# Optimization experiments

Hardware: AMD Instinct MI355X
Metric: run time of the kernel (lower is better)

## Reference

```python
import jax, jax.numpy as jnp
import numpy as np

NEG = -1e30  # finite stand-in for log(0); safe for logaddexp and its gradient


def setup_inputs() -> dict:
    key = jax.random.key(0)
    k1, k2 = jax.random.split(key)
    B, T, C, U = 256, 512, 128, 128
    logits = jax.random.normal(k1, (B, T, C), dtype=jnp.float32)
    y_pred = jax.nn.softmax(logits, axis=-1)  # ctc_batch_cost expects probabilities
    y_true = jax.random.randint(k2, (B, U), 0, C - 1)  # labels exclude blank=C-1
    return {"y_true": y_true, "y_pred": y_pred}


def _ctc_batch_cost(y_true, y_pred):
    """Keras-style CTC: blank = num_classes-1, logp = log(y_pred + 1e-7),
    full input_length = T and label_length = U for every row (as in the layer).
    Returns loss of shape [B, 1]."""
    B, T, C = y_pred.shape
    U = y_true.shape[1]
    blank = C - 1
    S = 2 * U + 1  # extended label: blank-interleaved
    logp = jnp.log(y_pred + 1e-7)  # [B,T,C], keras epsilon

    # extended label sequence z = [blank, l1, blank, l2, ..., lU, blank]
    ext = jnp.full((B, S), blank, dtype=y_true.dtype).at[:, 1::2].set(y_true)

    # lp[t,b,s] = logp[b,t,ext[b,s]]
    lp = jnp.take_along_axis(logp, jnp.broadcast_to(ext[:, None, :], (B, T, S)), axis=2)
    lp = jnp.transpose(lp, (1, 0, 2))  # [T,B,S]

    # skip transition s-2 -> s allowed iff z[s] != blank and z[s] != z[s-2]
    ext_m2 = jnp.pad(ext, ((0, 0), (2, 0)), constant_values=blank)[:, :S]
    skip = (ext != blank) & (ext != ext_m2)
    skip = skip.at[:, :2].set(False)  # no s-2 predecessor for s in {0,1}

    alpha0 = jnp.full((B, S), NEG, dtype=logp.dtype)
    alpha0 = alpha0.at[:, 0].set(lp[0, :, 0]).at[:, 1].set(lp[0, :, 1])

    def step(a, lp_t):
        a1 = jnp.pad(a, ((0, 0), (1, 0)), constant_values=NEG)[:, :S]
        a2 = jnp.pad(a, ((0, 0), (2, 0)), constant_values=NEG)[:, :S]
        a2 = jnp.where(skip, a2, NEG)
        a = jnp.logaddexp(jnp.logaddexp(a, a1), a2) + lp_t
        return a, None

    aT, _ = jax.lax.scan(step, alpha0, lp[1:])
    loss = -jnp.logaddexp(aT[:, S - 1], aT[:, S - 2])
    return loss[:, None]  # [B,1], matching ctc_batch_cost output shape


def reference(y_true, y_pred):
    # The layer returns y_pred and registers the loss via add_loss; the loss is
    # the actual computation of interest, so we return it.
    return _ctc_batch_cost(y_true, y_pred)
```

## Files before the change

kernel.cpp:

```cpp
#include <hip/hip_runtime.h>

#define EPSF 1e-7f

#define DPPF0(x, ctrl) \
    __int_as_float(__builtin_amdgcn_update_dpp(0, __float_as_int(x), ctrl, 0xF, 0xF, false))

__device__ __forceinline__ float f_rcp(float x) { return __builtin_amdgcn_rcpf(x); }
__device__ __forceinline__ float wave_shr1_f(float x) { return DPPF0(x, 0x138); }

__device__ __forceinline__ float wave_max64(float x) {
    x = fmaxf(x, DPPF0(x, 0x111));
    x = fmaxf(x, DPPF0(x, 0x112));
    x = fmaxf(x, DPPF0(x, 0x114));
    x = fmaxf(x, DPPF0(x, 0x118));
    x = fmaxf(x, DPPF0(x, 0x142));
    x = fmaxf(x, DPPF0(x, 0x143));
    return __int_as_float(__builtin_amdgcn_readlane(__float_as_int(x), 63));
}

#define SB0() __builtin_amdgcn_sched_barrier(0)
#define WAITV(N) do { asm volatile("s_waitcnt vmcnt(" #N ")" ::: "memory"); SB0(); } while (0)

#define ISS(dst, voff, IMM) \
    asm volatile("global_load_dword %0, %1, %2 offset:" #IMM \
                 : "=v"(dst) : "v"(voff), "s"(pn))

#define ISSUE_W8(X) do { \
    ISS(X##b[0], vb, 0);    ISS(X##l1[0], v1, 0);    ISS(X##l3[0], v3, 0); \
    ISS(X##b[1], vb, 512);  ISS(X##l1[1], v1, 512);  ISS(X##l3[1], v3, 512); \
    ISS(X##b[2], vb, 1024); ISS(X##l1[2], v1, 1024); ISS(X##l3[2], v3, 1024); \
    ISS(X##b[3], vb, 1536); ISS(X##l1[3], v1, 1536); ISS(X##l3[3], v3, 1536); \
    ISS(X##b[4], vb, 2048); ISS(X##l1[4], v1, 2048); ISS(X##l3[4], v3, 2048); \
    ISS(X##b[5], vb, 2560); ISS(X##l1[5], v1, 2560); ISS(X##l3[5], v3, 2560); \
    ISS(X##b[6], vb, 3072); ISS(X##l1[6], v1, 3072); ISS(X##l3[6], v3, 3072); \
    ISS(X##b[7], vb, 3584); ISS(X##l1[7], v1, 3584); ISS(X##l3[7], v3, 3584); \
    pn += 8 * 128; \
} while (0)

#define ISSUE_W7(X) do { \
    ISS(X##b[0], vb, 0);    ISS(X##l1[0], v1, 0);    ISS(X##l3[0], v3, 0); \
    ISS(X##b[1], vb, 512);  ISS(X##l1[1], v1, 512);  ISS(X##l3[1], v3, 512); \
    ISS(X##b[2], vb, 1024); ISS(X##l1[2], v1, 1024); ISS(X##l3[2], v3, 1024); \
    ISS(X##b[3], vb, 1536); ISS(X##l1[3], v1, 1536); ISS(X##l3[3], v3, 1536); \
    ISS(X##b[4], vb, 2048); ISS(X##l1[4], v1, 2048); ISS(X##l3[4], v3, 2048); \
    ISS(X##b[5], vb, 2560); ISS(X##l1[5], v1, 2560); ISS(X##l3[5], v3, 2560); \
    ISS(X##b[6], vb, 3072); ISS(X##l1[6], v1, 3072); ISS(X##l3[6], v3, 3072); \
} while (0)

#define STEP(PB_, P1_, P3_) do { \
    const float pbe = (PB_) + EPSF; \
    const float rpb = f_rcp(pbe); \
    const float q1  = ((P1_) + EPSF) * rpb; \
    const float q3  = ((P3_) + EPSF) * rpb; \
    const float n3  = wave_shr1_f(u3); \
    const float t1  = fmaf(m1, n3, u0 + u1); \
    const float t3  = fmaf(m3, u1, u2 + u3); \
    u4 = u4 + u3; \
    u3 = t3 * q3; \
    u2 = u2 + u1; \
    u1 = t1 * q1; \
    u0 = u0 + n3; \
    O += __logf(pbe); \
} while (0)

#define APPLY() do { \
    const float rm_ = f_rcp(m_carry); \
    u0 *= rm_; u1 *= rm_; u2 *= rm_; u3 *= rm_; u4 *= rm_; \
    O += __logf(m_carry); \
} while (0)

#define SNAP() do { \
    m_carry = wave_max64(fmaxf(fmaxf(u0, u1), fmaxf(u2, fmaxf(u3, u4)))); \
} while (0)

#define STEPK(X, k) STEP(X##b[k], X##l1[k], X##l3[k])
#define CONSUME_W8(X) do { \
    STEPK(X,0); STEPK(X,1); APPLY(); \
    STEPK(X,2); STEPK(X,3); STEPK(X,4); STEPK(X,5); STEPK(X,6); STEPK(X,7); \
    SNAP(); \
} while (0)
#define CONSUME_T7(X) do { \
    STEPK(X,0); STEPK(X,1); APPLY(); \
    STEPK(X,2); STEPK(X,3); STEPK(X,4); STEPK(X,5); STEPK(X,6); \
} while (0)

__global__ __launch_bounds__(64, 1) void ctc_pipe512(
        const int* __restrict__ y_true, const float* __restrict__ y_pred,
        float* __restrict__ out) {
    const int b    = blockIdx.x;
    const int lane = threadIdx.x;
    const float* __restrict__ yp = y_pred + (size_t)b * (512 * 128);

    const int2 lc = ((const int2*)(y_true + (size_t)b * 128))[lane];
    const int c1 = lc.x, c3 = lc.y;
    const int cp = __builtin_amdgcn_update_dpp(0, c3, 0x138, 0xF, 0xF, false);
    const float m1 = (lane > 0 && c1 != cp) ? 1.f : 0.f;
    const float m3 = (c3 != c1) ? 1.f : 0.f;

    float u0, u1, u2 = 0.f, u3 = 0.f, u4 = 0.f;
    {
        const float pvb = yp[127];
        const float pv1 = yp[c1];
        u0 = (lane == 0) ? pvb + EPSF : 0.f;
        u1 = (lane == 0) ? pv1 + EPSF : 0.f;
    }
    float O = 0.f, m_carry = 1.0f;

    const int vb = 127 * 4;
    const int v1 = c1 * 4;
    const int v3 = c3 * 4;
    const float* pn = yp + 128;

    WAITV(0);

    float Ab[8], Al1[8], Al3[8];
    float Bb[8], Bl1[8], Bl3[8];
    float Cb[8], Cl1[8], Cl3[8];

    ISSUE_W8(A);
    ISSUE_W8(B);

    for (int j = 0; j < 20; ++j) {
        ISSUE_W8(C);  WAITV(48);  CONSUME_W8(A);
        ISSUE_W8(A);  WAITV(48);  CONSUME_W8(B);
        ISSUE_W8(B);  WAITV(48);  CONSUME_W8(C);
    }
    ISSUE_W8(C);
    WAITV(48);  CONSUME_W8(A);
    ISSUE_W7(A);
    WAITV(45);  CONSUME_W8(B);
    WAITV(21);  CONSUME_W8(C);
    WAITV(0);   CONSUME_T7(A);

    if (lane == 63) out[b] = -(O + __logf(u3 + u4));
}

__global__ __launch_bounds__(64, 1) void ctc_scan_generic(
        const int* __restrict__ y_true, const float* __restrict__ y_pred,
        float* __restrict__ out, int T, int C, int U) {
    const int b    = blockIdx.x;
    const int lane = threadIdx.x;
    const int blank = C - 1;
    const float* __restrict__ yp = y_pred + (size_t)b * T * C;

    const int2 lc = ((const int2*)(y_true + (size_t)b * U))[lane];
    const int c1 = lc.x, c3 = lc.y;
    const int cp = __builtin_amdgcn_update_dpp(0, c3, 0x138, 0xF, 0xF, false);
    const float m1 = (lane > 0 && c1 != cp) ? 1.f : 0.f;
    const float m3 = (c3 != c1) ? 1.f : 0.f;

    float u0, u1, u2 = 0.f, u3 = 0.f, u4 = 0.f;
    u0 = (lane == 0) ? yp[blank] + EPSF : 0.f;
    u1 = (lane == 0) ? yp[c1] + EPSF : 0.f;
    float O = 0.f, m_carry = 1.0f;
    int kren = 0;

    for (int t = 1; t < T; ++t) {
        const float* row = yp + (size_t)t * C;
        STEP(row[blank], row[c1], row[c3]);
        if (++kren == 8) { SNAP(); APPLY(); kren = 0; }
    }
    if (lane == 63) out[b] = -(O + __logf(u3 + u4));
}

extern "C" void kernel_launch(void* const* d_in, const int* in_sizes, int n_in,
                              void* d_out, int out_size, void* d_ws, size_t ws_size,
                              hipStream_t stream) {
    const int*   y_true = (const int*)d_in[0];
    const float* y_pred = (const float*)d_in[1];
    float*       out    = (float*)d_out;

    const int B = out_size;
    const int U = in_sizes[0] / B;
    const int C = 128;
    const int T = in_sizes[1] / (B * C);

    if (T == 512 && C == 128 && U == 128) {
        ctc_pipe512<<<B, 64, 0, stream>>>(y_true, y_pred, out);
    } else {
        ctc_scan_generic<<<B, 64, 0, stream>>>(y_true, y_pred, out, T, C, U);
    }
}
```

Before: 45.11 us.

## Stage full probability rows into LDS via async global_load_lds triple buffer

Result: slower. 51.56 us (+14.3%).

```diff
diff --git a/kernel.cpp b/kernel.cpp
--- a/kernel.cpp
+++ b/kernel.cpp
@@ -21,31 +21,13 @@
 #define SB0() __builtin_amdgcn_sched_barrier(0)
 #define WAITV(N) do { asm volatile("s_waitcnt vmcnt(" #N ")" ::: "memory"); SB0(); } while (0)
 
-#define ISS(dst, voff, IMM) \
-    asm volatile("global_load_dword %0, %1, %2 offset:" #IMM \
-                 : "=v"(dst) : "v"(voff), "s"(pn))
-
-#define ISSUE_W8(X) do { \
-    ISS(X##b[0], vb, 0);    ISS(X##l1[0], v1, 0);    ISS(X##l3[0], v3, 0); \
-    ISS(X##b[1], vb, 512);  ISS(X##l1[1], v1, 512);  ISS(X##l3[1], v3, 512); \
-    ISS(X##b[2], vb, 1024); ISS(X##l1[2], v1, 1024); ISS(X##l3[2], v3, 1024); \
-    ISS(X##b[3], vb, 1536); ISS(X##l1[3], v1, 1536); ISS(X##l3[3], v3, 1536); \
-    ISS(X##b[4], vb, 2048); ISS(X##l1[4], v1, 2048); ISS(X##l3[4], v3, 2048); \
-    ISS(X##b[5], vb, 2560); ISS(X##l1[5], v1, 2560); ISS(X##l3[5], v3, 2560); \
-    ISS(X##b[6], vb, 3072); ISS(X##l1[6], v1, 3072); ISS(X##l3[6], v3, 3072); \
-    ISS(X##b[7], vb, 3584); ISS(X##l1[7], v1, 3584); ISS(X##l3[7], v3, 3584); \
-    pn += 8 * 128; \
-} while (0)
-
-#define ISSUE_W7(X) do { \
-    ISS(X##b[0], vb, 0);    ISS(X##l1[0], v1, 0);    ISS(X##l3[0], v3, 0); \
-    ISS(X##b[1], vb, 512);  ISS(X##l1[1], v1, 512);  ISS(X##l3[1], v3, 512); \
-    ISS(X##b[2], vb, 1024); ISS(X##l1[2], v1, 1024); ISS(X##l3[2], v3, 1024); \
-    ISS(X##b[3], vb, 1536); ISS(X##l1[3], v1, 1536); ISS(X##l3[3], v3, 1536); \
-    ISS(X##b[4], vb, 2048); ISS(X##l1[4], v1, 2048); ISS(X##l3[4], v3, 2048); \
-    ISS(X##b[5], vb, 2560); ISS(X##l1[5], v1, 2560); ISS(X##l3[5], v3, 2560); \
-    ISS(X##b[6], vb, 3072); ISS(X##l1[6], v1, 3072); ISS(X##l3[6], v3, 3072); \
-} while (0)
+__device__ __forceinline__ void stage8(const float* gsrc, float* lbuf, int lane) {
+    const char* g = (const char*)gsrc + lane * 16;
+    __builtin_amdgcn_global_load_lds((const void*)(g),        (void*)(lbuf),       16, 0, 0);
+    __builtin_amdgcn_global_load_lds((const void*)(g + 1024), (void*)(lbuf + 256), 16, 0, 0);
+    __builtin_amdgcn_global_load_lds((const void*)(g + 2048), (void*)(lbuf + 512), 16, 0, 0);
+    __builtin_amdgcn_global_load_lds((const void*)(g + 3072), (void*)(lbuf + 768), 16, 0, 0);
+}
 
 #define STEP(PB_, P1_, P3_) do { \
     const float pbe = (PB_) + EPSF; \
@@ -73,23 +55,28 @@
     m_carry = wave_max64(fmaxf(fmaxf(u0, u1), fmaxf(u2, fmaxf(u3, u4)))); \
 } while (0)
 
-#define STEPK(X, k) STEP(X##b[k], X##l1[k], X##l3[k])
-#define CONSUME_W8(X) do { \
-    STEPK(X,0); STEPK(X,1); APPLY(); \
-    STEPK(X,2); STEPK(X,3); STEPK(X,4); STEPK(X,5); STEPK(X,6); STEPK(X,7); \
+#define LDK(k) \
+    const float pb##k = R[k][127]; \
+    const float pA##k = R[k][c1]; \
+    const float pB##k = R[k][c3];
+
+#define CONS8(Q) do { \
+    const float (*R)[128] = lds[Q]; \
+    LDK(0) LDK(1) LDK(2) LDK(3) LDK(4) LDK(5) LDK(6) LDK(7) \
+    STEP(pb0, pA0, pB0); STEP(pb1, pA1, pB1); APPLY(); \
+    STEP(pb2, pA2, pB2); STEP(pb3, pA3, pB3); STEP(pb4, pA4, pB4); \
+    STEP(pb5, pA5, pB5); STEP(pb6, pA6, pB6); STEP(pb7, pA7, pB7); \
     SNAP(); \
 } while (0)
-#define CONSUME_T7(X) do { \
-    STEPK(X,0); STEPK(X,1); APPLY(); \
-    STEPK(X,2); STEPK(X,3); STEPK(X,4); STEPK(X,5); STEPK(X,6); \
-} while (0)
 
-__global__ __launch_bounds__(64, 1) void ctc_pipe512(
+__global__ __launch_bounds__(64, 1) void ctc_lds512(
         const int* __restrict__ y_true, const float* __restrict__ y_pred,
         float* __restrict__ out) {
     const int b    = blockIdx.x;
     const int lane = threadIdx.x;
     const float* __restrict__ yp = y_pred + (size_t)b * (512 * 128);
+
+    __shared__ float lds[4][8][128];
 
     const int2 lc = ((const int2*)(y_true + (size_t)b * 128))[lane];
     const int c1 = lc.x, c3 = lc.y;
@@ -106,31 +93,35 @@
     }
     float O = 0.f, m_carry = 1.0f;
 
-    const int vb = 127 * 4;
-    const int v1 = c1 * 4;
-    const int v3 = c3 * 4;
-    const float* pn = yp + 128;
-
     WAITV(0);
 
-    float Ab[8], Al1[8], Al3[8];
-    float Bb[8], Bl1[8], Bl3[8];
-    float Cb[8], Cl1[8], Cl3[8];
+    stage8(yp + 1 * 128,  &lds[0][0][0], lane);
+    stage8(yp + 9 * 128,  &lds[1][0][0], lane);
+    stage8(yp + 17 * 128, &lds[2][0][0], lane);
 
-    ISSUE_W8(A);
-    ISSUE_W8(B);
+    const float* gp = yp + 25 * 128;
 
+#pragma unroll 1
     for (int j = 0; j < 20; ++j) {
-        ISSUE_W8(C);  WAITV(48);  CONSUME_W8(A);
-        ISSUE_W8(A);  WAITV(48);  CONSUME_W8(B);
-        ISSUE_W8(B);  WAITV(48);  CONSUME_W8(C);
+        WAITV(8);  CONS8(0);  stage8(gp, &lds[0][0][0], lane);  gp += 1024;
+        WAITV(8);  CONS8(1);  stage8(gp, &lds[1][0][0], lane);  gp += 1024;
+        WAITV(8);  CONS8(2);  stage8(gp, &lds[2][0][0], lane);  gp += 1024;
     }
-    ISSUE_W8(C);
-    WAITV(48);  CONSUME_W8(A);
-    ISSUE_W7(A);
-    WAITV(45);  CONSUME_W8(B);
-    WAITV(21);  CONSUME_W8(C);
-    WAITV(0);   CONSUME_T7(A);
+    WAITV(8);  CONS8(0);  stage8(yp + 504 * 128, &lds[3][0][0], lane);
+    WAITV(8);  CONS8(1);
+    WAITV(4);  CONS8(2);
+    WAITV(0);
+    {
+        const float (*R)[128] = lds[3];
+        STEP(R[1][127], R[1][c1], R[1][c3]);
+        STEP(R[2][127], R[2][c1], R[2][c3]);
+        APPLY();
+        STEP(R[3][127], R[3][c1], R[3][c3]);
+        STEP(R[4][127], R[4][c1], R[4][c3]);
+        STEP(R[5][127], R[5][c1], R[5][c3]);
+        STEP(R[6][127], R[6][c1], R[6][c3]);
+        STEP(R[7][127], R[7][c1], R[7][c3]);
+    }
 
     if (lane == 63) out[b] = -(O + __logf(u3 + u4));
 }
@@ -176,7 +167,7 @@
     const int T = in_sizes[1] / (B * C);
 
     if (T == 512 && C == 128 && U == 128) {
-        ctc_pipe512<<<B, 64, 0, stream>>>(y_true, y_pred, out);
+        ctc_lds512<<<B, 64, 0, stream>>>(y_true, y_pred, out);
     } else {
         ctc_scan_generic<<<B, 64, 0, stream>>>(y_true, y_pred, out, T, C, U);
     }
```

## Load full probability rows coalesced and route label values via ds_bpermute

Applied to the files above, without the earlier changes.

Result: slower. 60.40 us (+33.9%).

```diff
diff --git a/kernel.cpp b/kernel.cpp
--- a/kernel.cpp
+++ b/kernel.cpp
@@ -1,6 +1,8 @@
 #include <hip/hip_runtime.h>
 
 #define EPSF 1e-7f
+
+typedef float f32x2 __attribute__((ext_vector_type(2)));
 
 #define DPPF0(x, ctrl) \
     __int_as_float(__builtin_amdgcn_update_dpp(0, __float_as_int(x), ctrl, 0xF, 0xF, false))
@@ -21,31 +23,29 @@
 #define SB0() __builtin_amdgcn_sched_barrier(0)
 #define WAITV(N) do { asm volatile("s_waitcnt vmcnt(" #N ")" ::: "memory"); SB0(); } while (0)
 
-#define ISS(dst, voff, IMM) \
-    asm volatile("global_load_dword %0, %1, %2 offset:" #IMM \
+#define ISS2(dst, IMM) \
+    asm volatile("global_load_dwordx2 %0, %1, %2 offset:" #IMM \
                  : "=v"(dst) : "v"(voff), "s"(pn))
 
 #define ISSUE_W8(X) do { \
-    ISS(X##b[0], vb, 0);    ISS(X##l1[0], v1, 0);    ISS(X##l3[0], v3, 0); \
-    ISS(X##b[1], vb, 512);  ISS(X##l1[1], v1, 512);  ISS(X##l3[1], v3, 512); \
-    ISS(X##b[2], vb, 1024); ISS(X##l1[2], v1, 1024); ISS(X##l3[2], v3, 1024); \
-    ISS(X##b[3], vb, 1536); ISS(X##l1[3], v1, 1536); ISS(X##l3[3], v3, 1536); \
-    ISS(X##b[4], vb, 2048); ISS(X##l1[4], v1, 2048); ISS(X##l3[4], v3, 2048); \
-    ISS(X##b[5], vb, 2560); ISS(X##l1[5], v1, 2560); ISS(X##l3[5], v3, 2560); \
-    ISS(X##b[6], vb, 3072); ISS(X##l1[6], v1, 3072); ISS(X##l3[6], v3, 3072); \
-    ISS(X##b[7], vb, 3584); ISS(X##l1[7], v1, 3584); ISS(X##l3[7], v3, 3584); \
+    ISS2(X[0], 0);    ISS2(X[1], 512);  ISS2(X[2], 1024); ISS2(X[3], 1536); \
+    ISS2(X[4], 2048); ISS2(X[5], 2560); ISS2(X[6], 3072); ISS2(X[7], 3584); \
     pn += 8 * 128; \
 } while (0)
 
-#define ISSUE_W7(X) do { \
-    ISS(X##b[0], vb, 0);    ISS(X##l1[0], v1, 0);    ISS(X##l3[0], v3, 0); \
-    ISS(X##b[1], vb, 512);  ISS(X##l1[1], v1, 512);  ISS(X##l3[1], v3, 512); \
-    ISS(X##b[2], vb, 1024); ISS(X##l1[2], v1, 1024); ISS(X##l3[2], v3, 1024); \
-    ISS(X##b[3], vb, 1536); ISS(X##l1[3], v1, 1536); ISS(X##l3[3], v3, 1536); \
-    ISS(X##b[4], vb, 2048); ISS(X##l1[4], v1, 2048); ISS(X##l3[4], v3, 2048); \
-    ISS(X##b[5], vb, 2560); ISS(X##l1[5], v1, 2560); ISS(X##l3[5], v3, 2560); \
-    ISS(X##b[6], vb, 3072); ISS(X##l1[6], v1, 3072); ISS(X##l3[6], v3, 3072); \
+#define ISSUE_T7(X) do { \
+    ISS2(X[0], 0);    ISS2(X[1], 512);  ISS2(X[2], 1024); ISS2(X[3], 1536); \
+    ISS2(X[4], 2048); ISS2(X[5], 2560); ISS2(X[6], 3072); \
 } while (0)
+
+#define ROUTE(X, k) \
+    const int px1_##k = __builtin_amdgcn_ds_bpermute(a1, __float_as_int(X[k].x)); \
+    const int py1_##k = __builtin_amdgcn_ds_bpermute(a1, __float_as_int(X[k].y)); \
+    const int px3_##k = __builtin_amdgcn_ds_bpermute(a3, __float_as_int(X[k].x)); \
+    const int py3_##k = __builtin_amdgcn_ds_bpermute(a3, __float_as_int(X[k].y)); \
+    const float pb_##k = __int_as_float(__builtin_amdgcn_readlane(__float_as_int(X[k].y), 63)); \
+    const float p1_##k = __int_as_float(sel1 ? py1_##k : px1_##k); \
+    const float p3_##k = __int_as_float(sel3 ? py3_##k : px3_##k);
 
 #define STEP(PB_, P1_, P3_) do { \
     const float pbe = (PB_) + EPSF; \
@@ -73,18 +73,24 @@
     m_carry = wave_max64(fmaxf(fmaxf(u0, u1), fmaxf(u2, fmaxf(u3, u4)))); \
 } while (0)
 
-#define STEPK(X, k) STEP(X##b[k], X##l1[k], X##l3[k])
-#define CONSUME_W8(X) do { \
-    STEPK(X,0); STEPK(X,1); APPLY(); \
-    STEPK(X,2); STEPK(X,3); STEPK(X,4); STEPK(X,5); STEPK(X,6); STEPK(X,7); \
+#define STEPK(k) STEP(pb_##k, p1_##k, p3_##k)
+
+#define CONS8(X) do { \
+    ROUTE(X,0) ROUTE(X,1) ROUTE(X,2) ROUTE(X,3) \
+    ROUTE(X,4) ROUTE(X,5) ROUTE(X,6) ROUTE(X,7) \
+    STEPK(0); STEPK(1); APPLY(); \
+    STEPK(2); STEPK(3); STEPK(4); STEPK(5); STEPK(6); STEPK(7); \
     SNAP(); \
 } while (0)
-#define CONSUME_T7(X) do { \
-    STEPK(X,0); STEPK(X,1); APPLY(); \
-    STEPK(X,2); STEPK(X,3); STEPK(X,4); STEPK(X,5); STEPK(X,6); \
+
+#define CONS_T7(X) do { \
+    ROUTE(X,0) ROUTE(X,1) ROUTE(X,2) ROUTE(X,3) \
+    ROUTE(X,4) ROUTE(X,5) ROUTE(X,6) \
+    STEPK(0); STEPK(1); APPLY(); \
+    STEPK(2); STEPK(3); STEPK(4); STEPK(5); STEPK(6); \
 } while (0)
 
-__global__ __launch_bounds__(64, 1) void ctc_pipe512(
+__global__ __launch_bounds__(64, 1) void ctc_bperm512(
         const int* __restrict__ y_true, const float* __restrict__ y_pred,
         float* __restrict__ out) {
     const int b    = blockIdx.x;
@@ -97,6 +103,11 @@
     const float m1 = (lane > 0 && c1 != cp) ? 1.f : 0.f;
     const float m3 = (c3 != c1) ? 1.f : 0.f;
 
+    const int  a1   = (c1 >> 1) << 2;
+    const int  a3   = (c3 >> 1) << 2;
+    const bool sel1 = (c1 & 1) != 0;
+    const bool sel3 = (c3 & 1) != 0;
+
     float u0, u1, u2 = 0.f, u3 = 0.f, u4 = 0.f;
     {
         const float pvb = yp[127];
@@ -106,31 +117,26 @@
     }
     float O = 0.f, m_carry = 1.0f;
 
-    const int vb = 127 * 4;
-    const int v1 = c1 * 4;
-    const int v3 = c3 * 4;
+    const int voff = lane * 8;
     const float* pn = yp + 128;
 
     WAITV(0);
 
-    float Ab[8], Al1[8], Al3[8];
-    float Bb[8], Bl1[8], Bl3[8];
-    float Cb[8], Cl1[8], Cl3[8];
-
+    f32x2 A[8], B[8], C[8];
     ISSUE_W8(A);
     ISSUE_W8(B);
 
     for (int j = 0; j < 20; ++j) {
-        ISSUE_W8(C);  WAITV(48);  CONSUME_W8(A);
-        ISSUE_W8(A);  WAITV(48);  CONSUME_W8(B);
-        ISSUE_W8(B);  WAITV(48);  CONSUME_W8(C);
+        ISSUE_W8(C);  WAITV(16);  CONS8(A);
+        ISSUE_W8(A);  WAITV(16);  CONS8(B);
+        ISSUE_W8(B);  WAITV(16);  CONS8(C);
     }
     ISSUE_W8(C);
-    WAITV(48);  CONSUME_W8(A);
-    ISSUE_W7(A);
-    WAITV(45);  CONSUME_W8(B);
-    WAITV(21);  CONSUME_W8(C);
-    WAITV(0);   CONSUME_T7(A);
+    WAITV(16);  CONS8(A);
+    ISSUE_T7(A);
+    WAITV(15);  CONS8(B);
+    WAITV(7);   CONS8(C);
+    WAITV(0);   CONS_T7(A);
 
     if (lane == 63) out[b] = -(O + __logf(u3 + u4));
 }
@@ -176,7 +182,7 @@
     const int T = in_sizes[1] / (B * C);
 
     if (T == 512 && C == 128 && U == 128) {
-        ctc_pipe512<<<B, 64, 0, stream>>>(y_true, y_pred, out);
+        ctc_bperm512<<<B, 64, 0, stream>>>(y_true, y_pred, out);
     } else {
         ctc_scan_generic<<<B, 64, 0, stream>>>(y_true, y_pred, out, T, C, U);
     }
```

## Drop per-step blank normalization and rescale every four steps with precomputed factors

Applied to the files above, without the earlier changes.

New measurement: 41.22 us. -8.6%, faster.

```diff
diff --git a/kernel.cpp b/kernel.cpp
--- a/kernel.cpp
+++ b/kernel.cpp
@@ -25,66 +25,86 @@
     asm volatile("global_load_dword %0, %1, %2 offset:" #IMM \
                  : "=v"(dst) : "v"(voff), "s"(pn))
 
-#define ISSUE_W8(X) do { \
-    ISS(X##b[0], vb, 0);    ISS(X##l1[0], v1, 0);    ISS(X##l3[0], v3, 0); \
-    ISS(X##b[1], vb, 512);  ISS(X##l1[1], v1, 512);  ISS(X##l3[1], v3, 512); \
-    ISS(X##b[2], vb, 1024); ISS(X##l1[2], v1, 1024); ISS(X##l3[2], v3, 1024); \
-    ISS(X##b[3], vb, 1536); ISS(X##l1[3], v1, 1536); ISS(X##l3[3], v3, 1536); \
-    ISS(X##b[4], vb, 2048); ISS(X##l1[4], v1, 2048); ISS(X##l3[4], v3, 2048); \
-    ISS(X##b[5], vb, 2560); ISS(X##l1[5], v1, 2560); ISS(X##l3[5], v3, 2560); \
-    ISS(X##b[6], vb, 3072); ISS(X##l1[6], v1, 3072); ISS(X##l3[6], v3, 3072); \
-    ISS(X##b[7], vb, 3584); ISS(X##l1[7], v1, 3584); ISS(X##l3[7], v3, 3584); \
+#define GISSUE(X) do { \
+    ISS(X##b[0], vb, 0);    ISS(X##1[0], v1, 0);    ISS(X##3[0], v3, 0); \
+    ISS(X##b[1], vb, 512);  ISS(X##1[1], v1, 512);  ISS(X##3[1], v3, 512); \
+    ISS(X##b[2], vb, 1024); ISS(X##1[2], v1, 1024); ISS(X##3[2], v3, 1024); \
+    ISS(X##b[3], vb, 1536); ISS(X##1[3], v1, 1536); ISS(X##3[3], v3, 1536); \
+    ISS(X##b[4], vb, 2048); ISS(X##1[4], v1, 2048); ISS(X##3[4], v3, 2048); \
+    ISS(X##b[5], vb, 2560); ISS(X##1[5], v1, 2560); ISS(X##3[5], v3, 2560); \
+    ISS(X##b[6], vb, 3072); ISS(X##1[6], v1, 3072); ISS(X##3[6], v3, 3072); \
+    ISS(X##b[7], vb, 3584); ISS(X##1[7], v1, 3584); ISS(X##3[7], v3, 3584); \
     pn += 8 * 128; \
 } while (0)
 
-#define ISSUE_W7(X) do { \
-    ISS(X##b[0], vb, 0);    ISS(X##l1[0], v1, 0);    ISS(X##l3[0], v3, 0); \
-    ISS(X##b[1], vb, 512);  ISS(X##l1[1], v1, 512);  ISS(X##l3[1], v3, 512); \
-    ISS(X##b[2], vb, 1024); ISS(X##l1[2], v1, 1024); ISS(X##l3[2], v3, 1024); \
-    ISS(X##b[3], vb, 1536); ISS(X##l1[3], v1, 1536); ISS(X##l3[3], v3, 1536); \
-    ISS(X##b[4], vb, 2048); ISS(X##l1[4], v1, 2048); ISS(X##l3[4], v3, 2048); \
-    ISS(X##b[5], vb, 2560); ISS(X##l1[5], v1, 2560); ISS(X##l3[5], v3, 2560); \
-    ISS(X##b[6], vb, 3072); ISS(X##l1[6], v1, 3072); ISS(X##l3[6], v3, 3072); \
-} while (0)
-
-#define STEP(PB_, P1_, P3_) do { \
-    const float pbe = (PB_) + EPSF; \
-    const float rpb = f_rcp(pbe); \
-    const float q1  = ((P1_) + EPSF) * rpb; \
-    const float q3  = ((P3_) + EPSF) * rpb; \
-    const float n3  = wave_shr1_f(u3); \
-    const float t1  = fmaf(m1, n3, u0 + u1); \
-    const float t3  = fmaf(m3, u1, u2 + u3); \
-    u4 = u4 + u3; \
-    u3 = t3 * q3; \
-    u2 = u2 + u1; \
-    u1 = t1 * q1; \
-    u0 = u0 + n3; \
-    O += __logf(pbe); \
-} while (0)
-
-#define APPLY() do { \
-    const float rm_ = f_rcp(m_carry); \
-    u0 *= rm_; u1 *= rm_; u2 *= rm_; u3 *= rm_; u4 *= rm_; \
-    O += __logf(m_carry); \
-} while (0)
-
-#define SNAP() do { \
-    m_carry = wave_max64(fmaxf(fmaxf(u0, u1), fmaxf(u2, fmaxf(u3, u4)))); \
-} while (0)
-
-#define STEPK(X, k) STEP(X##b[k], X##l1[k], X##l3[k])
-#define CONSUME_W8(X) do { \
-    STEPK(X,0); STEPK(X,1); APPLY(); \
-    STEPK(X,2); STEPK(X,3); STEPK(X,4); STEPK(X,5); STEPK(X,6); STEPK(X,7); \
-    SNAP(); \
-} while (0)
-#define CONSUME_T7(X) do { \
-    STEPK(X,0); STEPK(X,1); APPLY(); \
-    STEPK(X,2); STEPK(X,3); STEPK(X,4); STEPK(X,5); STEPK(X,6); \
-} while (0)
-
-__global__ __launch_bounds__(64, 1) void ctc_pipe512(
+#define GISSUE_T7(X) do { \
+    ISS(X##b[0], vb, 0);    ISS(X##1[0], v1, 0);    ISS(X##3[0], v3, 0); \
+    ISS(X##b[1], vb, 512);  ISS(X##1[1], v1, 512);  ISS(X##3[1], v3, 512); \
+    ISS(X##b[2], vb, 1024); ISS(X##1[2], v1, 1024); ISS(X##3[2], v3, 1024); \
+    ISS(X##b[3], vb, 1536); ISS(X##1[3], v1, 1536); ISS(X##3[3], v3, 1536); \
+    ISS(X##b[4], vb, 2048); ISS(X##1[4], v1, 2048); ISS(X##3[4], v3, 2048); \
+    ISS(X##b[5], vb, 2560); ISS(X##1[5], v1, 2560); ISS(X##3[5], v3, 2560); \
+    ISS(X##b[6], vb, 3072); ISS(X##1[6], v1, 3072); ISS(X##3[6], v3, 3072); \
+} while (0)
+
+#define PSTEP(PBE_, P1_, P3_) do { \
+    const float e1 = (P1_) + EPSF; \
+    const float e3 = (P3_) + EPSF; \
+    const float n3 = wave_shr1_f(u3); \
+    const float t1 = fmaf(m1, n3, u0 + u1); \
+    const float t3 = fmaf(m3, u1, u2 + u3); \
+    u4 = (u4 + u3) * (PBE_); \
+    u3 = t3 * e3; \
+    u2 = (u2 + u1) * (PBE_); \
+    u1 = t1 * e1; \
+    u0 = (u0 + n3) * (PBE_); \
+} while (0)
+
+#define SNAP(RM, LM) do { \
+    float mm_ = fmaxf(fmaxf(u0, u1), fmaxf(u2, fmaxf(u3, u4))); \
+    mm_ = wave_max64(mm_); \
+    RM = f_rcp(mm_); \
+    LM = __logf(mm_); \
+} while (0)
+
+#define APPLY(RM, LM) do { \
+    u0 *= RM; u1 *= RM; u2 *= RM; u3 *= RM; u4 *= RM; \
+    O += LM; \
+} while (0)
+
+#define PBE(X, k) const float pbe##k = X##b[k] + EPSF;
+
+#define CONS8(X) do { \
+    PBE(X,0) PBE(X,1) PBE(X,2) PBE(X,3) PBE(X,4) PBE(X,5) PBE(X,6) PBE(X,7) \
+    PSTEP(pbe0, X##1[0], X##3[0]); \
+    PSTEP(pbe1, X##1[1], X##3[1]); \
+    APPLY(rmA, lmA); \
+    PSTEP(pbe2, X##1[2], X##3[2]); \
+    PSTEP(pbe3, X##1[3], X##3[3]); \
+    SNAP(rmB, lmB); \
+    PSTEP(pbe4, X##1[4], X##3[4]); \
+    PSTEP(pbe5, X##1[5], X##3[5]); \
+    APPLY(rmB, lmB); \
+    PSTEP(pbe6, X##1[6], X##3[6]); \
+    PSTEP(pbe7, X##1[7], X##3[7]); \
+    SNAP(rmA, lmA); \
+} while (0)
+
+#define CONS_T7(X) do { \
+    PBE(X,0) PBE(X,1) PBE(X,2) PBE(X,3) PBE(X,4) PBE(X,5) PBE(X,6) \
+    PSTEP(pbe0, X##1[0], X##3[0]); \
+    PSTEP(pbe1, X##1[1], X##3[1]); \
+    APPLY(rmA, lmA); \
+    PSTEP(pbe2, X##1[2], X##3[2]); \
+    PSTEP(pbe3, X##1[3], X##3[3]); \
+    SNAP(rmB, lmB); \
+    PSTEP(pbe4, X##1[4], X##3[4]); \
+    PSTEP(pbe5, X##1[5], X##3[5]); \
+    APPLY(rmB, lmB); \
+    PSTEP(pbe6, X##1[6], X##3[6]); \
+} while (0)
+
+__global__ __launch_bounds__(64, 1) void ctc_prod512(
         const int* __restrict__ y_true, const float* __restrict__ y_pred,
         float* __restrict__ out) {
     const int b    = blockIdx.x;
@@ -104,7 +124,8 @@
         u0 = (lane == 0) ? pvb + EPSF : 0.f;
         u1 = (lane == 0) ? pv1 + EPSF : 0.f;
     }
-    float O = 0.f, m_carry = 1.0f;
+    float O = 0.f;
+    float rmA = 1.0f, lmA = 0.0f, rmB = 1.0f, lmB = 0.0f;
 
     const int vb = 127 * 4;
     const int v1 = c1 * 4;
@@ -113,24 +134,22 @@
 
     WAITV(0);
 
-    float Ab[8], Al1[8], Al3[8];
-    float Bb[8], Bl1[8], Bl3[8];
-    float Cb[8], Cl1[8], Cl3[8];
-
-    ISSUE_W8(A);
-    ISSUE_W8(B);
+    float Ab[8], A1[8], A3[8];
+    float Bb[8], B1[8], B3[8];
+    float Cb[8], C1[8], C3[8];
+
+    GISSUE(A);
+    GISSUE(B);
 
     for (int j = 0; j < 20; ++j) {
-        ISSUE_W8(C);  WAITV(48);  CONSUME_W8(A);
-        ISSUE_W8(A);  WAITV(48);  CONSUME_W8(B);
-        ISSUE_W8(B);  WAITV(48);  CONSUME_W8(C);
-    }
-    ISSUE_W8(C);
-    WAITV(48);  CONSUME_W8(A);
-    ISSUE_W7(A);
-    WAITV(45);  CONSUME_W8(B);
-    WAITV(21);  CONSUME_W8(C);
-    WAITV(0);   CONSUME_T7(A);
+        WAITV(24); GISSUE(C); CONS8(A);
+        WAITV(24); GISSUE(A); CONS8(B);
+        WAITV(24); GISSUE(B); CONS8(C);
+    }
+    WAITV(24); GISSUE(C);    CONS8(A);
+    WAITV(24); GISSUE_T7(A); CONS8(B);
+    WAITV(21); CONS8(C);
+    WAITV(0);  CONS_T7(A);
 
     if (lane == 63) out[b] = -(O + __logf(u3 + u4));
 }
@@ -152,13 +171,15 @@
     float u0, u1, u2 = 0.f, u3 = 0.f, u4 = 0.f;
     u0 = (lane == 0) ? yp[blank] + EPSF : 0.f;
     u1 = (lane == 0) ? yp[c1] + EPSF : 0.f;
-    float O = 0.f, m_carry = 1.0f;
+    float O = 0.f;
+    float rmA = 1.0f, lmA = 0.0f;
     int kren = 0;
 
     for (int t = 1; t < T; ++t) {
         const float* row = yp + (size_t)t * C;
-        STEP(row[blank], row[c1], row[c3]);
-        if (++kren == 8) { SNAP(); APPLY(); kren = 0; }
+        const float pbe = row[blank] + EPSF;
+        PSTEP(pbe, row[c1], row[c3]);
+        if (++kren == 4) { SNAP(rmA, lmA); APPLY(rmA, lmA); kren = 0; }
     }
     if (lane == 63) out[b] = -(O + __logf(u3 + u4));
 }
@@ -176,7 +197,7 @@
     const int T = in_sizes[1] / (B * C);
 
     if (T == 512 && C == 128 && U == 128) {
-        ctc_pipe512<<<B, 64, 0, stream>>>(y_true, y_pred, out);
+        ctc_prod512<<<B, 64, 0, stream>>>(y_true, y_pred, out);
     } else {
         ctc_scan_generic<<<B, 64, 0, stream>>>(y_true, y_pred, out, T, C, U);
     }
```
